# Optimization experiments

Measured on AMD Instinct MI355X. Metric: run time of the kernel, lower is better.

## Reference

```python
import jax, jax.numpy as jnp
import numpy as np
import math

B, S, E, H = 2, 2048, 768, 12
D = E // H            # head_dim = 64
FFN = 3072            # GeGLU hidden
WIN = 64              # local window size
GLOBAL_IDS = np.array([0])
EPS = 1e-5


def _rope(x):
    # x: [B,H,S,D]; interleaved rotary embedding, theta=10000 (lucidrains RotaryEmbedding)
    d = x.shape[-1]
    s = x.shape[-2]
    inv_freq = 1.0 / (10000.0 ** (jnp.arange(0, d, 2, dtype=jnp.float32) / d))
    freqs = jnp.arange(s, dtype=jnp.float32)[:, None] * inv_freq[None, :]  # [S, D/2]
    freqs = jnp.repeat(freqs, 2, axis=-1)                                   # [S, D]
    cos, sin = jnp.cos(freqs), jnp.sin(freqs)
    xp = x.reshape(x.shape[:-1] + (d // 2, 2))
    x_rot = jnp.stack([-xp[..., 1], xp[..., 0]], axis=-1).reshape(x.shape)
    return x * cos + x_rot * sin


def _layernorm(x, scale, bias):
    mu = jnp.mean(x, axis=-1, keepdims=True)
    var = jnp.mean(jnp.square(x - mu), axis=-1, keepdims=True)
    return (x - mu) * jax.lax.rsqrt(var + EPS) * scale + bias


def setup_inputs() -> dict:
    key = jax.random.key(0)
    ks = jax.random.split(key, 10)
    def xav(k, shape, gain):
        fan_out, fan_in = shape
        std = gain * math.sqrt(2.0 / (fan_in + fan_out))
        return jax.random.normal(k, shape, jnp.float32) * std
    g2 = math.sqrt(2.0)
    g13 = math.sqrt(1.0 / 3.0)
    return {
        "x": jax.random.normal(ks[0], (B, S, E), jnp.float32),
        "rel_pos_bias": jax.random.normal(ks[1], (B, S, S), jnp.float32),
        "mask": jnp.ones((B, S), dtype=bool),
        "wq_w": xav(ks[2], (E, E), g2), "wq_b": jnp.zeros((E,), jnp.float32),
        "wk_w": xav(ks[3], (E, E), g2), "wk_b": jnp.zeros((E,), jnp.float32),
        "wv_w": xav(ks[4], (E, E), g2), "wv_b": jnp.zeros((E,), jnp.float32),
        "fc_w": xav(ks[5], (E, E), g2), "fc_b": jnp.zeros((E,), jnp.float32),
        "pos_coeff": jnp.full((H, 1, 1), 0.01, jnp.float32),
        "gate_w": xav(ks[6], (FFN, E), g13), "gate_b": jnp.zeros((FFN,), jnp.float32),
        "value_w": xav(ks[7], (FFN, E), g2), "value_b": jnp.zeros((FFN,), jnp.float32),
        "down_w": xav(ks[8], (E, FFN), g2), "down_b": jnp.zeros((E,), jnp.float32),
        "ln1_s": jnp.ones((E,), jnp.float32), "ln1_b": jnp.zeros((E,), jnp.float32),
        "ln2_s": jnp.ones((E,), jnp.float32), "ln2_b": jnp.zeros((E,), jnp.float32),
    }


def _sparse_allow(mask):
    # static local-window + global-token pattern, [S,S] bool
    idx = jnp.arange(S)
    allow = jnp.abs(idx[:, None] - idx[None, :]) <= WIN
    gidx = jnp.asarray(GLOBAL_IDS)
    allow = allow.at[gidx, :].set(True)
    allow = allow.at[:, gidx].set(True)
    # combine with padding mask [B,S] broadcast over query rows
    return allow[None, None, :, :] & mask[:, None, None, :]  # [B,1,S,S]


def reference(x, rel_pos_bias, mask, wq_w, wq_b, wk_w, wk_b, wv_w, wv_b,
              fc_w, fc_b, pos_coeff, gate_w, gate_b, value_w, value_b,
              down_w, down_b, ln1_s, ln1_b, ln2_s, ln2_b):
    def heads(t):  # [B,S,E] -> [B,H,S,D]
        return t.reshape(B, S, H, D).transpose(0, 2, 1, 3)

    Q = _rope(heads(x @ wq_w.T + wq_b))
    K = _rope(heads(x @ wk_w.T + wk_b))
    V = heads(x @ wv_w.T + wv_b)

    scores = jnp.einsum('bhqd,bhkd->bhqk', Q, K) / math.sqrt(D)
    scores = scores + pos_coeff[None] * rel_pos_bias[:, None]     # [B,H,S,S]
    allow = _sparse_allow(mask)
    scores = jnp.where(allow, scores, -1e30)
    scores = scores - jnp.max(scores, axis=-1, keepdims=True)
    attn = jax.nn.softmax(scores, axis=-1)
    ctx = jnp.einsum('bhqk,bhkd->bhqd', attn, V)
    ctx = ctx.transpose(0, 2, 1, 3).reshape(B, S, E)
    attn_out = ctx @ fc_w.T + fc_b

    h = _layernorm(x + attn_out, ln1_s, ln1_b)
    gate = jax.nn.gelu(h @ gate_w.T + gate_b, approximate=False)
    ffn = (gate * (h @ value_w.T + value_b)) @ down_w.T + down_b
    return _layernorm(h + ffn, ln2_s, ln2_b)
```

## Files before the change

### kernel.cpp

```cpp
#include <hip/hip_runtime.h>
#include <math.h>

#define B_   2
#define S_   2048
#define E_   768
#define H_   12
#define D_   64
#define FFN_ 3072
#define WIN_ 64
#define MTOT (B_*S_)

typedef unsigned short ushort_t;
typedef unsigned short ushort8 __attribute__((ext_vector_type(8)));
typedef __bf16 bf16x8 __attribute__((ext_vector_type(8)));
typedef float f32x4 __attribute__((ext_vector_type(4)));
typedef _Float16 half_t;

__device__ __forceinline__ float b2f(ushort_t u) {
    union { unsigned int i; float f; } c; c.i = ((unsigned int)u) << 16; return c.f;
}
__device__ __forceinline__ ushort_t f2b(float f) {
    union { float f; unsigned int i; } c; c.f = f;
    unsigned int u = c.i;
    return (ushort_t)((u + 0x7fffu + ((u >> 16) & 1u)) >> 16);
}
__device__ __forceinline__ float gelu_f(float g) {
    return 0.5f * g * (1.f + erff(g * 0.70710678118654752440f));
}

typedef const __attribute__((address_space(1))) void* gptr_t;
typedef __attribute__((address_space(3))) void* lptr_t;
__device__ __forceinline__ void gload16(const void* g, void* l) {
    __builtin_amdgcn_global_load_lds((gptr_t)g,
        (lptr_t)(unsigned int)(unsigned long long)l, 16, 0, 0);
}

__global__ __launch_bounds__(256)
void cvt_f32_bf16(const float* __restrict__ in, ushort_t* __restrict__ out, int n8)
{
    const int idx = blockIdx.x * 256 + threadIdx.x;
    if (idx >= n8) return;
    const float4* p = (const float4*)(in + (size_t)idx * 8);
    const float4 a = p[0], b = p[1];
    ushort8 o;
    o[0]=f2b(a.x); o[1]=f2b(a.y); o[2]=f2b(a.z); o[3]=f2b(a.w);
    o[4]=f2b(b.x); o[5]=f2b(b.y); o[6]=f2b(b.z); o[7]=f2b(b.w);
    *(ushort8*)(out + (size_t)idx*8) = o;
}

__global__ __launch_bounds__(256)
void cvt_interleave(const float* __restrict__ gw, const float* __restrict__ vw,
                    ushort_t* __restrict__ out)
{
    const int idx = blockIdx.x*256 + threadIdx.x;
    const int R   = idx / 96, c8 = idx - R*96;
    const int blk = R >> 6, w = R & 63;
    const float* src = (w < 32 ? gw : vw) + (size_t)(blk*32 + (w & 31))*768 + c8*8;
    const float4 a = ((const float4*)src)[0], b = ((const float4*)src)[1];
    ushort8 o;
    o[0]=f2b(a.x); o[1]=f2b(a.y); o[2]=f2b(a.z); o[3]=f2b(a.w);
    o[4]=f2b(b.x); o[5]=f2b(b.y); o[6]=f2b(b.z); o[7]=f2b(b.w);
    *(ushort8*)(out + (size_t)idx*8) = o;
}

__global__ __launch_bounds__(256)
void rope_table(float2* __restrict__ ctab)
{
    const int idx = blockIdx.x*256 + threadIdx.x;
    if (idx >= S_*32) return;
    const int s = idx >> 5, i = idx & 31;
    const float inv = exp2f(-(float)i * (13.287712379549449f/32.0f));
    const float fr = (float)s * inv;
    ctab[idx] = make_float2(cosf(fr), sinf(fr));
}

__global__ __launch_bounds__(256)
void rope_apply(ushort_t* __restrict__ Qb, ushort_t* __restrict__ Kb,
                const float2* __restrict__ ctab)
{
    const int NP4 = MTOT*E_/8;
    int idx = blockIdx.x*256 + threadIdx.x;
    ushort_t* ptr = Qb;
    if (idx >= NP4) { ptr = Kb; idx -= NP4; if (idx >= NP4) return; }
    const size_t p0 = (size_t)idx * 4;
    const int e2 = (int)(p0 % (E_/2));
    const int s  = (int)((p0 / (E_/2)) % S_);
    const int i0 = e2 & 31;
    ushort8 v = *(ushort8*)(ptr + p0*2);
    ushort8 o;
#pragma unroll
    for (int t = 0; t < 4; ++t) {
        const float2 cs = ctab[s*32 + i0 + t];
        const float x0 = b2f(v[2*t]), x1 = b2f(v[2*t+1]);
        o[2*t]   = f2b(x0*cs.x - x1*cs.y);
        o[2*t+1] = f2b(x1*cs.x + x0*cs.y);
    }
    *(ushort8*)(ptr + p0*2) = o;
}

template<int EPI, int BN>
__global__ __launch_bounds__(256)
void gemm_mfma(const ushort_t* __restrict__ A,
               const ushort_t* W0, const float* b0, void* C0,
               const ushort_t* W1, const float* b1, void* C1,
               const ushort_t* W2, const float* b2, void* C2,
               const void* __restrict__ aux, int M, int N, int K)
{
    constexpr int NWC = BN/64, NWR = 4/NWC, WROWS = 128/NWR, MF = WROWS/16;
    const ushort_t* W = W0; const float* bias = b0; void* C = C0;
    if (blockIdx.z == 1) { W = W1; bias = b1; C = C1; }
    else if (blockIdx.z == 2) { W = W2; bias = b2; C = C2; }

    __shared__ __align__(16) ushort_t As[128*32];
    __shared__ __align__(16) ushort_t Bs[BN*32];

    const int tid = threadIdx.x, wv = tid>>6, lane = tid&63;
    const int m0 = blockIdx.y*128, n0 = blockIdx.x*BN;
    const int wr = wv / NWC, wc = wv % NWC;
    const int lr16 = lane & 15, lkb = (lane>>4)<<3;

    f32x4 acc[MF][4];
#pragma unroll
    for (int i=0;i<MF;++i)
#pragma unroll
        for (int j=0;j<4;++j) acc[i][j] = f32x4{0.f,0.f,0.f,0.f};

    const char* Ab = (const char*)(A + (size_t)m0*K);
    const char* Wb = (const char*)(W + (size_t)n0*K);
    const size_t rb = (size_t)K*2;
    const int wbase = wv*1024, lby = lane*16;

    for (int kt = 0; kt < K; kt += 32) {
        const size_t kb = (size_t)kt*2;
        int n_ = wbase + lby;
        gload16(Ab + (size_t)(n_>>6)*rb + kb + (n_&63), (char*)As + wbase);
        n_ += 4096;
        gload16(Ab + (size_t)(n_>>6)*rb + kb + (n_&63), (char*)As + wbase + 4096);
        n_ = wbase + lby;
        gload16(Wb + (size_t)(n_>>6)*rb + kb + (n_&63), (char*)Bs + wbase);
        if (BN == 128) {
            n_ += 4096;
            gload16(Wb + (size_t)(n_>>6)*rb + kb + (n_&63), (char*)Bs + wbase + 4096);
        }
        __syncthreads();
        bf16x8 af[MF], bfr[4];
#pragma unroll
        for (int mf=0; mf<MF; ++mf)
            af[mf] = *(const bf16x8*)&As[(wr*WROWS + mf*16 + lr16)*32 + lkb];
#pragma unroll
        for (int nf=0; nf<4; ++nf)
            bfr[nf] = *(const bf16x8*)&Bs[(wc*64 + nf*16 + lr16)*32 + lkb];
#pragma unroll
        for (int mf=0; mf<MF; ++mf)
#pragma unroll
            for (int nf=0; nf<4; ++nf)
                acc[mf][nf] = __builtin_amdgcn_mfma_f32_16x16x32_bf16(af[mf], bfr[nf], acc[mf][nf], 0,0,0);
        __syncthreads();
    }

    const int colb = n0 + wc*64 + lr16;
    const int rowb = m0 + wr*WROWS + ((lane>>4)<<2);
#pragma unroll
    for (int nf=0; nf<4; ++nf) {
        const int col = colb + nf*16;
        const float bsv = bias[col];
#pragma unroll
        for (int mf=0; mf<MF; ++mf) {
            const int row = rowb + mf*16;
            const f32x4 a = acc[mf][nf];
#pragma unroll
            for (int r=0; r<4; ++r) {
                const size_t off = (size_t)(row+r)*N + col;
                const float v = a[r] + bsv;
                if constexpr (EPI == 0) {
                    ((ushort_t*)C)[off] = f2b(v);
                } else if constexpr (EPI == 1) {
                    ((float*)C)[off] = v + ((const float*)aux)[off];
                } else {
                    if (blockIdx.z == 2) {
                        const int rr = row + r;
                        const size_t toff =
                            (((size_t)(rr >> 11)*H_ + (col >> 6))*64 + (col & 63))*(size_t)S_ + (rr & (S_-1));
                        ((ushort_t*)C)[toff] = f2b(v);
                    } else {
                        ((ushort_t*)C)[off] = f2b(v);
                    }
                }
            }
        }
    }
}

__global__ __launch_bounds__(512, 2)
void gemm_geglu(const ushort_t* __restrict__ A,
                const ushort_t* __restrict__ Wgv,
                const float* __restrict__ bgp,
                const float* __restrict__ bvp,
                ushort_t* __restrict__ C)
{
    constexpr int NT   = 12;
    constexpr int ABY  = 256*128;
    constexpr int BBY  = 128*128;
    constexpr int BUFB = ABY + BBY;
    __shared__ __align__(16) char lds[3*BUFB];

    const int id  = blockIdx.x;
    const int loc = id >> 3;
    const int gy  = loc / 6;
    const int gx  = (id & 7)*6 + (loc % 6);
    const int m0 = gy*256, n0 = gx*128;

    const int tid = threadIdx.x, wv = tid>>6, l = tid&63;
    const int wr = wv>>1, wc = wv&1;
    const int lr16 = l & 15, g16b = (l>>4)<<4;
    const int xr = (lr16 & 7) << 4;

    const int lrow = l >> 3;
    const int swzc = ((l & 7) ^ lrow) << 4;
    const char* Agp = (const char*)A   + (size_t)(m0 + wv*32 + lrow)*1536 + swzc;
    const char* Bgp = (const char*)Wgv + (size_t)(n0 + wv*16 + lrow)*1536 + swzc;

    const int rA0 = (wr*64 +  0 + lr16)*128, rA1 = (wr*64 + 16 + lr16)*128;
    const int rA2 = (wr*64 + 32 + lr16)*128, rA3 = (wr*64 + 48 + lr16)*128;
    const int rB0 = ABY + (wc*64 +  0 + lr16)*128, rB1 = ABY + (wc*64 + 16 + lr16)*128;
    const int rB2 = ABY + (wc*64 + 32 + lr16)*128, rB3 = ABY + (wc*64 + 48 + lr16)*128;
    const int ck0 = g16b ^ xr, ck1 = (64 + g16b) ^ xr;

    f32x4 acc[4][4];
#pragma unroll
    for (int i=0;i<4;++i)
#pragma unroll
        for (int j=0;j<4;++j) acc[i][j] = f32x4{0.f,0.f,0.f,0.f};

#define STG(tt, cb) { \
    char* dA = lds + (cb)*BUFB + wv*4096; \
    char* dB = lds + (cb)*BUFB + ABY + wv*2048; \
    const size_t ko = (size_t)(tt)*128; \
    gload16(Agp + ko,           dA); \
    gload16(Agp + ko +  8*1536, dA + 1024); \
    gload16(Agp + ko + 16*1536, dA + 2048); \
    gload16(Agp + ko + 24*1536, dA + 3072); \
    gload16(Bgp + ko,           dB); \
    gload16(Bgp + ko +  8*1536, dB + 1024); }

    STG(0, 0);
    STG(1, 1);
    asm volatile("s_waitcnt vmcnt(6)" ::: "memory");
    __builtin_amdgcn_s_barrier();

    int c = 0;
#pragma unroll 1
    for (int t = 0; t < NT; ++t) {
        const char* Lb = lds + c*BUFB;
        const int cs = (c==0) ? 2 : c-1;

        const bf16x8 a0 = *(const bf16x8*)(Lb + rA0 + ck0);
        const bf16x8 a1 = *(const bf16x8*)(Lb + rA1 + ck0);
        const bf16x8 a2 = *(const bf16x8*)(Lb + rA2 + ck0);
        const bf16x8 a3 = *(const bf16x8*)(Lb + rA3 + ck0);
        const bf16x8 b0 = *(const bf16x8*)(Lb + rB0 + ck0);
        const bf16x8 b1 = *(const bf16x8*)(Lb + rB1 + ck0);
        const bf16x8 b2 = *(const bf16x8*)(Lb + rB2 + ck0);
        const bf16x8 b3 = *(const bf16x8*)(Lb + rB3 + ck0);
        const bf16x8 e0 = *(const bf16x8*)(Lb + rA0 + ck1);
        const bf16x8 e1 = *(const bf16x8*)(Lb + rA1 + ck1);
        const bf16x8 e2 = *(const bf16x8*)(Lb + rA2 + ck1);
        const bf16x8 e3 = *(const bf16x8*)(Lb + rA3 + ck1);
        const bf16x8 f0 = *(const bf16x8*)(Lb + rB0 + ck1);
        const bf16x8 f1 = *(const bf16x8*)(Lb + rB1 + ck1);
        const bf16x8 f2 = *(const bf16x8*)(Lb + rB2 + ck1);
        const bf16x8 f3 = *(const bf16x8*)(Lb + rB3 + ck1);

        if (t < NT-2) STG(t+2, cs);

        __builtin_amdgcn_s_setprio(1);
        acc[0][0] = __builtin_amdgcn_mfma_f32_16x16x32_bf16(a0, b0, acc[0][0], 0,0,0);
        acc[1][0] = __builtin_amdgcn_mfma_f32_16x16x32_bf16(a1, b0, acc[1][0], 0,0,0);
        acc[2][0] = __builtin_amdgcn_mfma_f32_16x16x32_bf16(a2, b0, acc[2][0], 0,0,0);
        acc[3][0] = __builtin_amdgcn_mfma_f32_16x16x32_bf16(a3, b0, acc[3][0], 0,0,0);
        acc[0][1] = __builtin_amdgcn_mfma_f32_16x16x32_bf16(a0, b1, acc[0][1], 0,0,0);
        acc[1][1] = __builtin_amdgcn_mfma_f32_16x16x32_bf16(a1, b1, acc[1][1], 0,0,0);
        acc[2][1] = __builtin_amdgcn_mfma_f32_16x16x32_bf16(a2, b1, acc[2][1], 0,0,0);
        acc[3][1] = __builtin_amdgcn_mfma_f32_16x16x32_bf16(a3, b1, acc[3][1], 0,0,0);
        acc[0][2] = __builtin_amdgcn_mfma_f32_16x16x32_bf16(a0, b2, acc[0][2], 0,0,0);
        acc[1][2] = __builtin_amdgcn_mfma_f32_16x16x32_bf16(a1, b2, acc[1][2], 0,0,0);
        acc[2][2] = __builtin_amdgcn_mfma_f32_16x16x32_bf16(a2, b2, acc[2][2], 0,0,0);
        acc[3][2] = __builtin_amdgcn_mfma_f32_16x16x32_bf16(a3, b2, acc[3][2], 0,0,0);
        acc[0][3] = __builtin_amdgcn_mfma_f32_16x16x32_bf16(a0, b3, acc[0][3], 0,0,0);
        acc[1][3] = __builtin_amdgcn_mfma_f32_16x16x32_bf16(a1, b3, acc[1][3], 0,0,0);
        acc[2][3] = __builtin_amdgcn_mfma_f32_16x16x32_bf16(a2, b3, acc[2][3], 0,0,0);
        acc[3][3] = __builtin_amdgcn_mfma_f32_16x16x32_bf16(a3, b3, acc[3][3], 0,0,0);
        acc[0][0] = __builtin_amdgcn_mfma_f32_16x16x32_bf16(e0, f0, acc[0][0], 0,0,0);
        acc[1][0] = __builtin_amdgcn_mfma_f32_16x16x32_bf16(e1, f0, acc[1][0], 0,0,0);
        acc[2][0] = __builtin_amdgcn_mfma_f32_16x16x32_bf16(e2, f0, acc[2][0], 0,0,0);
        acc[3][0] = __builtin_amdgcn_mfma_f32_16x16x32_bf16(e3, f0, acc[3][0], 0,0,0);
        acc[0][1] = __builtin_amdgcn_mfma_f32_16x16x32_bf16(e0, f1, acc[0][1], 0,0,0);
        acc[1][1] = __builtin_amdgcn_mfma_f32_16x16x32_bf16(e1, f1, acc[1][1], 0,0,0);
        acc[2][1] = __builtin_amdgcn_mfma_f32_16x16x32_bf16(e2, f1, acc[2][1], 0,0,0);
        acc[3][1] = __builtin_amdgcn_mfma_f32_16x16x32_bf16(e3, f1, acc[3][1], 0,0,0);
        acc[0][2] = __builtin_amdgcn_mfma_f32_16x16x32_bf16(e0, f2, acc[0][2], 0,0,0);
        acc[1][2] = __builtin_amdgcn_mfma_f32_16x16x32_bf16(e1, f2, acc[1][2], 0,0,0);
        acc[2][2] = __builtin_amdgcn_mfma_f32_16x16x32_bf16(e2, f2, acc[2][2], 0,0,0);
        acc[3][2] = __builtin_amdgcn_mfma_f32_16x16x32_bf16(e3, f2, acc[3][2], 0,0,0);
        acc[0][3] = __builtin_amdgcn_mfma_f32_16x16x32_bf16(e0, f3, acc[0][3], 0,0,0);
        acc[1][3] = __builtin_amdgcn_mfma_f32_16x16x32_bf16(e1, f3, acc[1][3], 0,0,0);
        acc[2][3] = __builtin_amdgcn_mfma_f32_16x16x32_bf16(e2, f3, acc[2][3], 0,0,0);
        acc[3][3] = __builtin_amdgcn_mfma_f32_16x16x32_bf16(e3, f3, acc[3][3], 0,0,0);
        __builtin_amdgcn_s_setprio(0);

        if (t < NT-2)       { asm volatile("s_waitcnt vmcnt(6)" ::: "memory"); }
        else if (t == NT-2) { asm volatile("s_waitcnt vmcnt(0)" ::: "memory"); }
        if (t < NT-1) __builtin_amdgcn_s_barrier();

        c = (c==2) ? 0 : c+1;
    }
#undef STG

    const int colb = gx*64 + wc*32 + lr16;
    const int rowb = m0 + wr*64 + ((l>>4)<<2);
#pragma unroll
    for (int nf=0; nf<2; ++nf) {
        const int col = colb + nf*16;
        const float bgv = bgp[col], bvv = bvp[col];
#pragma unroll
        for (int mf=0; mf<4; ++mf) {
            const int row = rowb + mf*16;
            const f32x4 gq = acc[mf][nf];
            const f32x4 vq = acc[mf][nf+2];
#pragma unroll
            for (int r=0; r<4; ++r) {
                C[(size_t)(row+r)*3072 + col] =
                    f2b(gelu_f(gq[r] + bgv) * (vq[r] + bvv));
            }
        }
    }
}

__global__ __launch_bounds__(256, 3)
void gemm_down(const ushort_t* __restrict__ A,
               const ushort_t* __restrict__ Wd,
               const float* __restrict__ bias,
               float* __restrict__ P0,
               half_t* __restrict__ P1)
{
    constexpr int NT   = 24;
    constexpr int ABY  = 128*128;
    constexpr int BBY  = 64*128;
    constexpr int BUFB = ABY + BBY;
    __shared__ __align__(16) char lds[2*BUFB];

    const int id   = blockIdx.x;
    const int work = (id & 7)*96 + (id >> 3);
    const int z    = work / 384;
    const int r    = work - z*384;
    const int gy   = r / 12, gx = r - gy*12;
    const int m0 = gy*128, n0 = gx*64;

    const int tid = threadIdx.x, wv = tid>>6, l = tid&63;
    const int wr = wv>>1, wc = wv&1;
    const int lr16 = l & 15, g16b = (l>>4)<<4;
    const int xr = (lr16 & 7) << 4;

    const int lrow = l >> 3;
    const int swzc = ((l & 7) ^ lrow) << 4;
    const size_t kbase = (size_t)z*3072;
    const char* Agp = (const char*)A  + (size_t)(m0 + wv*32 + lrow)*6144 + kbase + swzc;
    const char* Bgp = (const char*)Wd + (size_t)(n0 + wv*16 + lrow)*6144 + kbase + swzc;

    const int rA0 = (wr*64 +  0 + lr16)*128, rA1 = (wr*64 + 16 + lr16)*128;
    const int rA2 = (wr*64 + 32 + lr16)*128, rA3 = (wr*64 + 48 + lr16)*128;
    const int rB0 = ABY + (wc*32 +  0 + lr16)*128;
    const int rB1 = ABY + (wc*32 + 16 + lr16)*128;
    const int ck0 = g16b ^ xr, ck1 = (64 + g16b) ^ xr;

    f32x4 acc[4][2];
#pragma unroll
    for (int i=0;i<4;++i)
#pragma unroll
        for (int j=0;j<2;++j) acc[i][j] = f32x4{0.f,0.f,0.f,0.f};

#define STGD(tt, cb) { \
    char* dA = lds + (cb)*BUFB + wv*4096; \
    char* dB = lds + (cb)*BUFB + ABY + wv*2048; \
    const size_t ko = (size_t)(tt)*128; \
    gload16(Agp + ko,           dA); \
    gload16(Agp + ko +  8*6144, dA + 1024); \
    gload16(Agp + ko + 16*6144, dA + 2048); \
    gload16(Agp + ko + 24*6144, dA + 3072); \
    gload16(Bgp + ko,           dB); \
    gload16(Bgp + ko +  8*6144, dB + 1024); }

    STGD(0, 0);
    __syncthreads();

    int c = 0;
#pragma unroll 1
    for (int t = 0; t < NT; ++t) {
        if (t < NT-1) STGD(t+1, c^1);
        const char* Lb = lds + c*BUFB;
        const bf16x8 a0 = *(const bf16x8*)(Lb + rA0 + ck0);
        const bf16x8 a1 = *(const bf16x8*)(Lb + rA1 + ck0);
        const bf16x8 a2 = *(const bf16x8*)(Lb + rA2 + ck0);
        const bf16x8 a3 = *(const bf16x8*)(Lb + rA3 + ck0);
        const bf16x8 b0 = *(const bf16x8*)(Lb + rB0 + ck0);
        const bf16x8 b1 = *(const bf16x8*)(Lb + rB1 + ck0);
        const bf16x8 e0 = *(const bf16x8*)(Lb + rA0 + ck1);
        const bf16x8 e1 = *(const bf16x8*)(Lb + rA1 + ck1);
        const bf16x8 e2 = *(const bf16x8*)(Lb + rA2 + ck1);
        const bf16x8 e3 = *(const bf16x8*)(Lb + rA3 + ck1);
        const bf16x8 f0 = *(const bf16x8*)(Lb + rB0 + ck1);
        const bf16x8 f1 = *(const bf16x8*)(Lb + rB1 + ck1);
        __builtin_amdgcn_s_setprio(1);
        acc[0][0] = __builtin_amdgcn_mfma_f32_16x16x32_bf16(a0, b0, acc[0][0], 0,0,0);
        acc[1][0] = __builtin_amdgcn_mfma_f32_16x16x32_bf16(a1, b0, acc[1][0], 0,0,0);
        acc[2][0] = __builtin_amdgcn_mfma_f32_16x16x32_bf16(a2, b0, acc[2][0], 0,0,0);
        acc[3][0] = __builtin_amdgcn_mfma_f32_16x16x32_bf16(a3, b0, acc[3][0], 0,0,0);
        acc[0][1] = __builtin_amdgcn_mfma_f32_16x16x32_bf16(a0, b1, acc[0][1], 0,0,0);
        acc[1][1] = __builtin_amdgcn_mfma_f32_16x16x32_bf16(a1, b1, acc[1][1], 0,0,0);
        acc[2][1] = __builtin_amdgcn_mfma_f32_16x16x32_bf16(a2, b1, acc[2][1], 0,0,0);
        acc[3][1] = __builtin_amdgcn_mfma_f32_16x16x32_bf16(a3, b1, acc[3][1], 0,0,0);
        acc[0][0] = __builtin_amdgcn_mfma_f32_16x16x32_bf16(e0, f0, acc[0][0], 0,0,0);
        acc[1][0] = __builtin_amdgcn_mfma_f32_16x16x32_bf16(e1, f0, acc[1][0], 0,0,0);
        acc[2][0] = __builtin_amdgcn_mfma_f32_16x16x32_bf16(e2, f0, acc[2][0], 0,0,0);
        acc[3][0] = __builtin_amdgcn_mfma_f32_16x16x32_bf16(e3, f0, acc[3][0], 0,0,0);
        acc[0][1] = __builtin_amdgcn_mfma_f32_16x16x32_bf16(e0, f1, acc[0][1], 0,0,0);
        acc[1][1] = __builtin_amdgcn_mfma_f32_16x16x32_bf16(e1, f1, acc[1][1], 0,0,0);
        acc[2][1] = __builtin_amdgcn_mfma_f32_16x16x32_bf16(e2, f1, acc[2][1], 0,0,0);
        acc[3][1] = __builtin_amdgcn_mfma_f32_16x16x32_bf16(e3, f1, acc[3][1], 0,0,0);
        __builtin_amdgcn_s_setprio(0);
        __syncthreads();
        c ^= 1;
    }
#undef STGD

    const int colb = n0 + wc*32 + lr16;
    const int rowb = m0 + wr*64 + ((l>>4)<<2);
#pragma unroll
    for (int nf=0; nf<2; ++nf) {
        const int col = colb + nf*16;
        const float bsv = bias[col];
#pragma unroll
        for (int mf=0; mf<4; ++mf) {
            const int row = rowb + mf*16;
            const f32x4 a = acc[mf][nf];
#pragma unroll
            for (int rr=0; rr<4; ++rr) {
                const size_t off = (size_t)(row+rr)*E_ + col;
                if (z == 0) P0[off] = a[rr] + bsv;
                else        P1[off] = (half_t)a[rr];
            }
        }
    }
}

__global__ __launch_bounds__(256)
void attn_mfma(const ushort_t* __restrict__ Qb, const ushort_t* __restrict__ Kb,
               const ushort_t* __restrict__ Vt, const float* __restrict__ rel,
               const float* __restrict__ pos_coeff, ushort_t* __restrict__ ctx)
{
    __shared__ __align__(16) ushort_t P_lds[4][16][160];
    const int id = blockIdx.x;
    const int h  = id % H_;
    const int qb = (id / H_) & 31;
    const int b  = id / (H_*32);
    const int wv = threadIdx.x >> 6, l = threadIdx.x & 63;
    const int qw = qb*64 + wv*16;
    const int g  = l >> 4, ql = l & 15;
    const int q  = qw + ql;

    int klo = qw - 64;
    if (klo < 0) klo = 0;
    if (klo > S_-160) klo = S_-160;
    const bool addg = (klo > 0);
    const float pc = pos_coeff[h];

    const ushort_t* qbp = Qb + ((size_t)(b*S_ + qw))*E_ + h*D_ + (size_t)ql*E_ + g*8;
    const bf16x8 qf0 = *(const bf16x8*)(qbp);
    const bf16x8 qf1 = *(const bf16x8*)(qbp + 32);

    float sg = -1e30f, pg = 0.f;
    const float* relrow = rel + ((size_t)(b*S_ + q))*S_;
    if (addg) {
        const ushort_t* k0p = Kb + (size_t)(b*S_)*E_ + h*D_ + g*8;
        const bf16x8 k00 = *(const bf16x8*)(k0p);
        const bf16x8 k01 = *(const bf16x8*)(k0p + 32);
        float part = 0.f;
#pragma unroll
        for (int t = 0; t < 8; ++t) {
            part = fmaf((float)k00[t], (float)qf0[t], part);
            part = fmaf((float)k01[t], (float)qf1[t], part);
        }
        part += __shfl_xor(part, 16);
        part += __shfl_xor(part, 32);
        sg = part*0.125f + pc*relrow[0];
    }

    f32x4 sc_[10];
#pragma unroll
    for (int f = 0; f < 10; ++f) sc_[f] = f32x4{0.f,0.f,0.f,0.f};
    const ushort_t* kbp = Kb + ((size_t)(b*S_ + klo))*E_ + h*D_;
#pragma unroll
    for (int f = 0; f < 10; ++f) {
        const ushort_t* kr = kbp + (size_t)(16*f + ql)*E_ + g*8;
        const bf16x8 kf0 = *(const bf16x8*)(kr);
        const bf16x8 kf1 = *(const bf16x8*)(kr + 32);
        sc_[f] = __builtin_amdgcn_mfma_f32_16x16x32_bf16(kf0, qf0, sc_[f], 0,0,0);
        sc_[f] = __builtin_amdgcn_mfma_f32_16x16x32_bf16(kf1, qf1, sc_[f], 0,0,0);
    }

#pragma unroll
    for (int f = 0; f < 10; ++f) {
#pragma unroll
        for (int r = 0; r < 4; ++r) {
            const int slot = 16*f + 4*g + r;
            const int key  = klo + slot;
            const int dd   = key - q;
            const bool ok  = (dd <= WIN_ && dd >= -WIN_) || (key == 0);
            const float v  = sc_[f][r]*0.125f + pc*relrow[key];
            sc_[f][r] = ok ? v : -1e30f;
        }
    }

    float mx = sg;
#pragma unroll
    for (int f = 0; f < 10; ++f)
#pragma unroll
        for (int r = 0; r < 4; ++r) mx = fmaxf(mx, sc_[f][r]);
    mx = fmaxf(mx, __shfl_xor(mx, 16));
    mx = fmaxf(mx, __shfl_xor(mx, 32));

    float ls = 0.f;
#pragma unroll
    for (int f = 0; f < 10; ++f)
#pragma unroll
        for (int r = 0; r < 4; ++r) {
            const float p = __expf(sc_[f][r] - mx);
            sc_[f][r] = p; ls += p;
        }
    if (addg) pg = __expf(sg - mx);
    ls += (g == 0) ? pg : 0.f;
    ls += __shfl_xor(ls, 16);
    ls += __shfl_xor(ls, 32);
    const float inv = 1.f / ls;

#pragma unroll
    for (int f = 0; f < 10; ++f)
#pragma unroll
        for (int r = 0; r < 4; ++r)
            P_lds[wv][ql][16*f + 4*g + r] = f2b(sc_[f][r]);
    __syncthreads();

    f32x4 acc_c[4];
#pragma unroll
    for (int df = 0; df < 4; ++df) acc_c[df] = f32x4{0.f,0.f,0.f,0.f};
    const ushort_t* vtb = Vt + ((size_t)(b*H_ + h)*64)*(size_t)S_;
#pragma unroll
    for (int s5 = 0; s5 < 5; ++s5) {
        const bf16x8 pf = *(const bf16x8*)&P_lds[wv][ql][32*s5 + 8*g];
#pragma unroll
        for (int df = 0; df < 4; ++df) {
            const bf16x8 vtf = *(const bf16x8*)(vtb + (size_t)(df*16 + ql)*S_ + klo + 32*s5 + g*8);
            acc_c[df] = __builtin_amdgcn_mfma_f32_16x16x32_bf16(vtf, pf, acc_c[df], 0,0,0);
        }
    }

    if (addg) {
#pragma unroll
        for (int df = 0; df < 4; ++df)
#pragma unroll
            for (int r = 0; r < 4; ++r)
                acc_c[df][r] = fmaf(pg, b2f(vtb[(size_t)(df*16 + g*4 + r)*S_]), acc_c[df][r]);
    }

    if (q != 0) {
        ushort_t* cb = ctx + ((size_t)(b*S_ + q))*E_ + h*D_;
#pragma unroll
        for (int df = 0; df < 4; ++df)
#pragma unroll
            for (int r = 0; r < 4; ++r)
                cb[df*16 + g*4 + r] = f2b(acc_c[df][r] * inv);
    }
}

__global__ __launch_bounds__(256)
void attn_global(const ushort_t* __restrict__ Qb, const ushort_t* __restrict__ Kb,
                 const ushort_t* __restrict__ Vt, const float* __restrict__ rel,
                 const float* __restrict__ pos_coeff, ushort_t* __restrict__ ctx)
{
    __shared__ float sc[S_];
    __shared__ float sq[D_];
    __shared__ float red[4];
    __shared__ float pacc[4][D_];
    const int tid = threadIdx.x, wv = tid>>6, lane = tid&63;
    const int id = blockIdx.x, h = id % H_, b = id / H_;

    if (tid < 64) sq[tid] = b2f(Qb[(size_t)(b*S_)*E_ + h*D_ + tid]);
    __syncthreads();

    const float pc = pos_coeff[h];
    const ushort_t* kbase = Kb + (size_t)b*S_*E_ + h*D_;
    const float* relrow = rel + (size_t)b*S_*S_;
    const int g = lane >> 2, sl = lane & 3;

    for (int jb = wv*16; jb < S_; jb += 64) {
        const int j = jb + g;
        const ushort_t* kr = kbase + (size_t)j*E_ + sl*16;
        const ushort8 k0 = *(const ushort8*)kr;
        const ushort8 k1 = *(const ushort8*)(kr + 8);
        const float* qv = &sq[sl*16];
        float partial = 0.f;
#pragma unroll
        for (int t = 0; t < 8; ++t) partial = fmaf(b2f(k0[t]), qv[t], partial);
#pragma unroll
        for (int t = 0; t < 8; ++t) partial = fmaf(b2f(k1[t]), qv[t+8], partial);
        partial += __shfl_xor(partial, 1);
        partial += __shfl_xor(partial, 2);
        if (sl == 0) sc[j] = partial*0.125f + pc*relrow[j];
    }
    __syncthreads();

    float mx = -1e30f;
#pragma unroll
    for (int i = 0; i < 8; ++i) mx = fmaxf(mx, sc[tid + 256*i]);
#pragma unroll
    for (int off = 32; off > 0; off >>= 1) mx = fmaxf(mx, __shfl_xor(mx, off));
    if (lane == 0) red[wv] = mx;
    __syncthreads();
    mx = fmaxf(fmaxf(red[0], red[1]), fmaxf(red[2], red[3]));

    float sum = 0.f;
#pragma unroll
    for (int i = 0; i < 8; ++i) {
        const float p = __expf(sc[tid + 256*i] - mx);
        sc[tid + 256*i] = p; sum += p;
    }
#pragma unroll
    for (int off = 32; off > 0; off >>= 1) sum += __shfl_xor(sum, off);
    __syncthreads();
    if (lane == 0) red[wv] = sum;
    __syncthreads();
    const float inv = 1.f / (red[0]+red[1]+red[2]+red[3]);

    const ushort_t* vtrow = Vt + ((size_t)(b*H_ + h)*64 + lane)*(size_t)S_;
    float acc = 0.f;
    for (int j0 = wv*512; j0 < wv*512 + 512; j0 += 8) {
        const ushort8 v8 = *(const ushort8*)&vtrow[j0];
#pragma unroll
        for (int t = 0; t < 8; ++t) acc = fmaf(sc[j0+t], b2f(v8[t]), acc);
    }
    pacc[wv][lane] = acc;
    __syncthreads();
    if (tid < 64) {
        const float r = (pacc[0][tid]+pacc[1][tid]+pacc[2][tid]+pacc[3][tid]) * inv;
        ctx[(size_t)(b*S_)*E_ + h*D_ + tid] = f2b(r);
    }
}

template<bool WB>
__global__ __launch_bounds__(256)
void ln_kernel(const float* __restrict__ in, const float* __restrict__ gam,
               const float* __restrict__ bet, float* __restrict__ out,
               ushort_t* __restrict__ outb)
{
    const int row = blockIdx.x;
    const float* r = in + (size_t)row * E_;
    const int tid = threadIdx.x;
    const float v0 = r[tid], v1 = r[tid+256], v2 = r[tid+512];
    float s  = v0+v1+v2;
    float ss = v0*v0+v1*v1+v2*v2;
#pragma unroll
    for (int off = 32; off > 0; off >>= 1) {
        s  += __shfl_xor(s, off);
        ss += __shfl_xor(ss, off);
    }
    __shared__ float rs[4], rss[4];
    const int wv = tid >> 6, lane = tid & 63;
    if (lane == 0) { rs[wv] = s; rss[wv] = ss; }
    __syncthreads();
    s  = rs[0]+rs[1]+rs[2]+rs[3];
    ss = rss[0]+rss[1]+rss[2]+rss[3];
    const float mu  = s * (1.f/E_);
    const float var = ss * (1.f/E_) - mu*mu;
    const float rstd = rsqrtf(var + 1e-5f);
    float* o = out + (size_t)row * E_;
    const float o0 = (v0-mu)*rstd*gam[tid    ] + bet[tid    ];
    const float o1 = (v1-mu)*rstd*gam[tid+256] + bet[tid+256];
    const float o2 = (v2-mu)*rstd*gam[tid+512] + bet[tid+512];
    o[tid] = o0; o[tid+256] = o1; o[tid+512] = o2;
    if constexpr (WB) {
        ushort_t* ob = outb + (size_t)row * E_;
        ob[tid] = f2b(o0); ob[tid+256] = f2b(o1); ob[tid+512] = f2b(o2);
    }
}

__global__ __launch_bounds__(256)
void ln3_kernel(const float* __restrict__ p0, const half_t* __restrict__ p1,
                const float* __restrict__ res, const float* __restrict__ gam,
                const float* __restrict__ bet, float* __restrict__ out)
{
    const int row = blockIdx.x;
    const size_t base = (size_t)row * E_;
    const int tid = threadIdx.x;
    const float v0 = p0[base+tid]     + (float)p1[base+tid]     + res[base+tid];
    const float v1 = p0[base+tid+256] + (float)p1[base+tid+256] + res[base+tid+256];
    const float v2 = p0[base+tid+512] + (float)p1[base+tid+512] + res[base+tid+512];
    float s  = v0+v1+v2;
    float ss = v0*v0+v1*v1+v2*v2;
#pragma unroll
    for (int off = 32; off > 0; off >>= 1) {
        s  += __shfl_xor(s, off);
        ss += __shfl_xor(ss, off);
    }
    __shared__ float rs[4], rss[4];
    const int wv = tid >> 6, lane = tid & 63;
    if (lane == 0) { rs[wv] = s; rss[wv] = ss; }
    __syncthreads();
    s  = rs[0]+rs[1]+rs[2]+rs[3];
    ss = rss[0]+rss[1]+rss[2]+rss[3];
    const float mu  = s * (1.f/E_);
    const float var = ss * (1.f/E_) - mu*mu;
    const float rstd = rsqrtf(var + 1e-5f);
    float* o = out + base;
    o[tid]     = (v0-mu)*rstd*gam[tid    ] + bet[tid    ];
    o[tid+256] = (v1-mu)*rstd*gam[tid+256] + bet[tid+256];
    o[tid+512] = (v2-mu)*rstd*gam[tid+512] + bet[tid+512];
}

extern "C" void kernel_launch(void* const* d_in, const int* in_sizes, int n_in,
                              void* d_out, int out_size, void* d_ws, size_t ws_size,
                              hipStream_t stream)
{
    const float* x      = (const float*)d_in[0];
    const float* rel    = (const float*)d_in[1];
    const float* wq_w   = (const float*)d_in[3];
    const float* wq_b   = (const float*)d_in[4];
    const float* wk_w   = (const float*)d_in[5];
    const float* wk_b   = (const float*)d_in[6];
    const float* wv_w   = (const float*)d_in[7];
    const float* wv_b   = (const float*)d_in[8];
    const float* fc_w   = (const float*)d_in[9];
    const float* fc_b   = (const float*)d_in[10];
    const float* pos_c  = (const float*)d_in[11];
    const float* gate_w = (const float*)d_in[12];
    const float* gate_b = (const float*)d_in[13];
    const float* value_w= (const float*)d_in[14];
    const float* value_b= (const float*)d_in[15];
    const float* down_w = (const float*)d_in[16];
    const float* down_b = (const float*)d_in[17];
    const float* ln1_s  = (const float*)d_in[18];
    const float* ln1_b  = (const float*)d_in[19];
    const float* ln2_s  = (const float*)d_in[20];
    const float* ln2_b  = (const float*)d_in[21];
    float* out = (float*)d_out;

    char* W = (char*)d_ws;
    ushort_t* Qb     = (ushort_t*)(W + 0);
    ushort_t* Kb     = (ushort_t*)(W + 6291456);
    ushort_t* Vt     = (ushort_t*)(W + 12582912);
    ushort_t* Cxb    = (ushort_t*)(W + 18874368);
    ushort_t* GpB    = (ushort_t*)(W + 0);
    ushort_t* Xb     = (ushort_t*)(W + 25165824);
    ushort_t* wqb    = (ushort_t*)(W + 31457280);
    ushort_t* wkb    = (ushort_t*)(W + 32636928);
    ushort_t* wvb    = (ushort_t*)(W + 33816576);
    ushort_t* fcb    = (ushort_t*)(W + 34996224);
    ushort_t* Wgv    = (ushort_t*)(W + 25165824);
    ushort_t* downb  = (ushort_t*)(W + 34996224);
    float*    AO     = (float*)   (W + 39714816);
    float*    Hb     = (float*)   (W + 52297728);
    ushort_t* Hbb    = (ushort_t*)(W + 64880640);
    half_t*   P1h    = (half_t*)  (W + 64880640);
    float2*   ctab   = (float2*)  (W + 71172096);

    cvt_f32_bf16<<<1536, 256, 0, stream>>>(x, Xb, MTOT*E_/8);
    cvt_f32_bf16<<<288,  256, 0, stream>>>(wq_w, wqb, E_*E_/8);
    cvt_f32_bf16<<<288,  256, 0, stream>>>(wk_w, wkb, E_*E_/8);
    cvt_f32_bf16<<<288,  256, 0, stream>>>(wv_w, wvb, E_*E_/8);
    cvt_f32_bf16<<<288,  256, 0, stream>>>(fc_w, fcb, E_*E_/8);
    rope_table<<<(S_*32+255)/256, 256, 0, stream>>>(ctab);

    gemm_mfma<2,128><<<dim3(E_/128, MTOT/128, 3), 256, 0, stream>>>(
        Xb, wqb, wq_b, Qb, wkb, wk_b, Kb, wvb, wv_b, Vt, nullptr, MTOT, E_, E_);

    cvt_interleave<<<2304, 256, 0, stream>>>(gate_w, value_w, Wgv);

    rope_apply<<<3072, 256, 0, stream>>>(Qb, Kb, ctab);

    attn_mfma<<<B_*H_*(S_/64), 256, 0, stream>>>(Qb, Kb, Vt, rel, pos_c, Cxb);
    attn_global<<<B_*H_, 256, 0, stream>>>(Qb, Kb, Vt, rel, pos_c, Cxb);

    gemm_mfma<1,64><<<dim3(E_/64, MTOT/128, 1), 256, 0, stream>>>(
        Cxb, fcb, fc_b, AO, nullptr, nullptr, nullptr, nullptr, nullptr, nullptr,
        x, MTOT, E_, E_);

    cvt_f32_bf16<<<1152, 256, 0, stream>>>(down_w, downb, E_*FFN_/8);

    ln_kernel<true><<<MTOT, 256, 0, stream>>>(AO, ln1_s, ln1_b, Hb, Hbb);

    gemm_geglu<<<dim3(768), 512, 0, stream>>>(Hbb, Wgv, gate_b, value_b, GpB);

    gemm_down<<<dim3(768), 256, 0, stream>>>(GpB, downb, down_b, AO, P1h);

    ln3_kernel<<<MTOT, 256, 0, stream>>>(AO, P1h, Hb, ln2_s, ln2_b, out);
}
```

Before: 237.5 us.

## Retile GeGLU GEMM to 128x128 blocks with 256 threads and K=32 stages

Changes the GeGLU projection GEMM from 256x128 tiles with 512 threads and 128-byte K slices to 128x128 tiles with 256 threads and 64-byte K slices, doubling the grid to 1536 blocks with a new swizzled block-to-tile mapping. LDS per block shrinks so three blocks can fit per CU, aiming for better occupancy and latency hiding. The price is twice as many barriers per K, less reuse per loaded tile, and a new LDS swizzle pattern.

Result: slower. 243.2 us (+2.4%).

```diff
diff --git a/kernel.cpp b/kernel.cpp
--- a/kernel.cpp
+++ b/kernel.cpp
@@ -191,40 +191,39 @@
     }
 }
 
-__global__ __launch_bounds__(512, 2)
+__global__ __launch_bounds__(256, 3)
 void gemm_geglu(const ushort_t* __restrict__ A,
                 const ushort_t* __restrict__ Wgv,
                 const float* __restrict__ bgp,
                 const float* __restrict__ bvp,
                 ushort_t* __restrict__ C)
 {
-    constexpr int NT   = 12;
-    constexpr int ABY  = 256*128;
-    constexpr int BBY  = 128*128;
-    constexpr int BUFB = ABY + BBY;
+    constexpr int NT   = 24;
+    constexpr int ABY  = 128*64;
+    constexpr int BUFB = 2*ABY;
     __shared__ __align__(16) char lds[3*BUFB];
 
     const int id  = blockIdx.x;
-    const int loc = id >> 3;
-    const int gy  = loc / 6;
-    const int gx  = (id & 7)*6 + (loc % 6);
-    const int m0 = gy*256, n0 = gx*128;
+    const int stI = (id & 7)*3 + ((id >> 3) >> 6);
+    const int w64 = (id >> 3) & 63;
+    const int gy  = (stI/6)*8 + (w64 >> 3);
+    const int gx  = (stI%6)*8 + (w64 & 7);
+    const int m0 = gy*128, n0 = gx*128;
 
     const int tid = threadIdx.x, wv = tid>>6, l = tid&63;
     const int wr = wv>>1, wc = wv&1;
-    const int lr16 = l & 15, g16b = (l>>4)<<4;
-    const int xr = (lr16 & 7) << 4;
-
-    const int lrow = l >> 3;
-    const int swzc = ((l & 7) ^ lrow) << 4;
-    const char* Agp = (const char*)A   + (size_t)(m0 + wv*32 + lrow)*1536 + swzc;
-    const char* Bgp = (const char*)Wgv + (size_t)(n0 + wv*16 + lrow)*1536 + swzc;
-
-    const int rA0 = (wr*64 +  0 + lr16)*128, rA1 = (wr*64 + 16 + lr16)*128;
-    const int rA2 = (wr*64 + 32 + lr16)*128, rA3 = (wr*64 + 48 + lr16)*128;
-    const int rB0 = ABY + (wc*64 +  0 + lr16)*128, rB1 = ABY + (wc*64 + 16 + lr16)*128;
-    const int rB2 = ABY + (wc*64 + 32 + lr16)*128, rB3 = ABY + (wc*64 + 48 + lr16)*128;
-    const int ck0 = g16b ^ xr, ck1 = (64 + g16b) ^ xr;
+    const int lr16 = l & 15;
+    const int ck = (((l>>4) ^ ((lr16>>1)&3)) << 4);
+
+    const int lr4   = l >> 2;
+    const int sslot = ((l & 3) ^ ((l >> 3) & 3)) << 4;
+    const char* Agp = (const char*)A   + (size_t)(m0 + wv*32 + lr4)*1536 + sslot;
+    const char* Bgp = (const char*)Wgv + (size_t)(n0 + wv*32 + lr4)*1536 + sslot;
+
+    const int rA0 = (wr*64 +  0 + lr16)*64, rA1 = (wr*64 + 16 + lr16)*64;
+    const int rA2 = (wr*64 + 32 + lr16)*64, rA3 = (wr*64 + 48 + lr16)*64;
+    const int rB0 = ABY + (wc*64 +  0 + lr16)*64, rB1 = ABY + (wc*64 + 16 + lr16)*64;
+    const int rB2 = ABY + (wc*64 + 32 + lr16)*64, rB3 = ABY + (wc*64 + 48 + lr16)*64;
 
     f32x4 acc[4][4];
 #pragma unroll
@@ -233,19 +232,17 @@
         for (int j=0;j<4;++j) acc[i][j] = f32x4{0.f,0.f,0.f,0.f};
 
 #define STG(tt, cb) { \
-    char* dA = lds + (cb)*BUFB + wv*4096; \
+    char* dA = lds + (cb)*BUFB + wv*2048; \
     char* dB = lds + (cb)*BUFB + ABY + wv*2048; \
-    const size_t ko = (size_t)(tt)*128; \
+    const size_t ko = (size_t)(tt)*64; \
     gload16(Agp + ko,           dA); \
-    gload16(Agp + ko +  8*1536, dA + 1024); \
-    gload16(Agp + ko + 16*1536, dA + 2048); \
-    gload16(Agp + ko + 24*1536, dA + 3072); \
+    gload16(Agp + ko + 16*1536, dA + 1024); \
     gload16(Bgp + ko,           dB); \
-    gload16(Bgp + ko +  8*1536, dB + 1024); }
+    gload16(Bgp + ko + 16*1536, dB + 1024); }
 
     STG(0, 0);
     STG(1, 1);
-    asm volatile("s_waitcnt vmcnt(6)" ::: "memory");
+    asm volatile("s_waitcnt vmcnt(4)" ::: "memory");
     __builtin_amdgcn_s_barrier();
 
     int c = 0;
@@ -254,22 +251,14 @@
         const char* Lb = lds + c*BUFB;
         const int cs = (c==0) ? 2 : c-1;
 
-        const bf16x8 a0 = *(const bf16x8*)(Lb + rA0 + ck0);
-        const bf16x8 a1 = *(const bf16x8*)(Lb + rA1 + ck0);
-        const bf16x8 a2 = *(const bf16x8*)(Lb + rA2 + ck0);
-        const bf16x8 a3 = *(const bf16x8*)(Lb + rA3 + ck0);
-        const bf16x8 b0 = *(const bf16x8*)(Lb + rB0 + ck0);
-        const bf16x8 b1 = *(const bf16x8*)(Lb + rB1 + ck0);
-        const bf16x8 b2 = *(const bf16x8*)(Lb + rB2 + ck0);
-        const bf16x8 b3 = *(const bf16x8*)(Lb + rB3 + ck0);
-        const bf16x8 e0 = *(const bf16x8*)(Lb + rA0 + ck1);
-        const bf16x8 e1 = *(const bf16x8*)(Lb + rA1 + ck1);
-        const bf16x8 e2 = *(const bf16x8*)(Lb + rA2 + ck1);
-        const bf16x8 e3 = *(const bf16x8*)(Lb + rA3 + ck1);
-        const bf16x8 f0 = *(const bf16x8*)(Lb + rB0 + ck1);
-        const bf16x8 f1 = *(const bf16x8*)(Lb + rB1 + ck1);
-        const bf16x8 f2 = *(const bf16x8*)(Lb + rB2 + ck1);
-        const bf16x8 f3 = *(const bf16x8*)(Lb + rB3 + ck1);
+        const bf16x8 a0 = *(const bf16x8*)(Lb + rA0 + ck);
+        const bf16x8 a1 = *(const bf16x8*)(Lb + rA1 + ck);
+        const bf16x8 a2 = *(const bf16x8*)(Lb + rA2 + ck);
+        const bf16x8 a3 = *(const bf16x8*)(Lb + rA3 + ck);
+        const bf16x8 b0 = *(const bf16x8*)(Lb + rB0 + ck);
+        const bf16x8 b1 = *(const bf16x8*)(Lb + rB1 + ck);
+        const bf16x8 b2 = *(const bf16x8*)(Lb + rB2 + ck);
+        const bf16x8 b3 = *(const bf16x8*)(Lb + rB3 + ck);
 
         if (t < NT-2) STG(t+2, cs);
 
@@ -290,25 +279,9 @@
         acc[1][3] = __builtin_amdgcn_mfma_f32_16x16x32_bf16(a1, b3, acc[1][3], 0,0,0);
         acc[2][3] = __builtin_amdgcn_mfma_f32_16x16x32_bf16(a2, b3, acc[2][3], 0,0,0);
         acc[3][3] = __builtin_amdgcn_mfma_f32_16x16x32_bf16(a3, b3, acc[3][3], 0,0,0);
-        acc[0][0] = __builtin_amdgcn_mfma_f32_16x16x32_bf16(e0, f0, acc[0][0], 0,0,0);
-        acc[1][0] = __builtin_amdgcn_mfma_f32_16x16x32_bf16(e1, f0, acc[1][0], 0,0,0);
-        acc[2][0] = __builtin_amdgcn_mfma_f32_16x16x32_bf16(e2, f0, acc[2][0], 0,0,0);
-        acc[3][0] = __builtin_amdgcn_mfma_f32_16x16x32_bf16(e3, f0, acc[3][0], 0,0,0);
-        acc[0][1] = __builtin_amdgcn_mfma_f32_16x16x32_bf16(e0, f1, acc[0][1], 0,0,0);
-        acc[1][1] = __builtin_amdgcn_mfma_f32_16x16x32_bf16(e1, f1, acc[1][1], 0,0,0);
-        acc[2][1] = __builtin_amdgcn_mfma_f32_16x16x32_bf16(e2, f1, acc[2][1], 0,0,0);
-        acc[3][1] = __builtin_amdgcn_mfma_f32_16x16x32_bf16(e3, f1, acc[3][1], 0,0,0);
-        acc[0][2] = __builtin_amdgcn_mfma_f32_16x16x32_bf16(e0, f2, acc[0][2], 0,0,0);
-        acc[1][2] = __builtin_amdgcn_mfma_f32_16x16x32_bf16(e1, f2, acc[1][2], 0,0,0);
-        acc[2][2] = __builtin_amdgcn_mfma_f32_16x16x32_bf16(e2, f2, acc[2][2], 0,0,0);
-        acc[3][2] = __builtin_amdgcn_mfma_f32_16x16x32_bf16(e3, f2, acc[3][2], 0,0,0);
-        acc[0][3] = __builtin_amdgcn_mfma_f32_16x16x32_bf16(e0, f3, acc[0][3], 0,0,0);
-        acc[1][3] = __builtin_amdgcn_mfma_f32_16x16x32_bf16(e1, f3, acc[1][3], 0,0,0);
-        acc[2][3] = __builtin_amdgcn_mfma_f32_16x16x32_bf16(e2, f3, acc[2][3], 0,0,0);
-        acc[3][3] = __builtin_amdgcn_mfma_f32_16x16x32_bf16(e3, f3, acc[3][3], 0,0,0);
         __builtin_amdgcn_s_setprio(0);
 
-        if (t < NT-2)       { asm volatile("s_waitcnt vmcnt(6)" ::: "memory"); }
+        if (t < NT-2)       { asm volatile("s_waitcnt vmcnt(4)" ::: "memory"); }
         else if (t == NT-2) { asm volatile("s_waitcnt vmcnt(0)" ::: "memory"); }
         if (t < NT-1) __builtin_amdgcn_s_barrier();
 
@@ -797,7 +770,7 @@
 
     ln_kernel<true><<<MTOT, 256, 0, stream>>>(AO, ln1_s, ln1_b, Hb, Hbb);
 
-    gemm_geglu<<<dim3(768), 512, 0, stream>>>(Hbb, Wgv, gate_b, value_b, GpB);
+    gemm_geglu<<<dim3(1536), 256, 0, stream>>>(Hbb, Wgv, gate_b, value_b, GpB);
 
     gemm_down<<<dim3(768), 256, 0, stream>>>(GpB, downb, down_b, AO, P1h);
 
```
